# Kernel tuning notes

Hardware: AMD Instinct MI355X
Metric: run time of the kernel (lower is better)

## Reference

```python
import jax, jax.numpy as jnp
import numpy as np

NUM_EMBEDDINGS = 4096
EMBEDDING_DIM = 256
COMMITMENT_COST = 0.25
N_TOKENS = 32768


def setup_inputs() -> dict:
    key = jax.random.key(0)
    k1, k2 = jax.random.split(key)
    inputs = jax.random.normal(k1, (N_TOKENS, EMBEDDING_DIM), dtype=jnp.float32)
    # torch init: uniform(-1/K, 1/K)
    lim = 1.0 / NUM_EMBEDDINGS
    weight = jax.random.uniform(k2, (NUM_EMBEDDINGS, EMBEDDING_DIM), dtype=jnp.float32,
                                minval=-lim, maxval=lim)
    return {"inputs": inputs, "weight": weight}


def reference(inputs, weight):
    distances = (jnp.sum(inputs ** 2, axis=1, keepdims=True)
                 + jnp.sum(weight ** 2, axis=1)
                 - 2.0 * jnp.matmul(inputs, weight.T))
    encoding_indices = jnp.argmin(distances, axis=1)                       # [N]
    encodings = jax.nn.one_hot(encoding_indices, NUM_EMBEDDINGS,
                               dtype=jnp.float32)                          # [N, K]
    # gather replaces onehot @ weight (same values)
    quantized = weight[encoding_indices]                                   # [N, D]

    commitment_loss = jnp.mean((jax.lax.stop_gradient(quantized) - inputs) ** 2)
    codebook_loss = jnp.mean((quantized - jax.lax.stop_gradient(inputs)) ** 2)
    loss = codebook_loss + COMMITMENT_COST * commitment_loss

    # straight-through estimator
    quantized_st = inputs + jax.lax.stop_gradient(quantized - inputs)

    avg_probs = jnp.mean(encodings, axis=0)                                # [K]
    perplexity = jnp.exp(-jnp.sum(avg_probs * jnp.log(avg_probs + 1e-10)))

    return (quantized_st, perplexity, encodings, encoding_indices, loss)
```

## Files before the change

kernel.cpp:

```cpp
#include <hip/hip_runtime.h>

#define N_TOK 32768
#define N_EMB 4096
#define DIM 256
#define NSTEP 128

typedef short bf16x8 __attribute__((ext_vector_type(8)));
typedef float f32x4 __attribute__((ext_vector_type(4)));
typedef unsigned short us8 __attribute__((ext_vector_type(8)));


static __device__ __forceinline__ unsigned short f2bf(float f) {
    unsigned int u = __float_as_uint(f);
    u = (u + 0x7fffu + ((u >> 16) & 1u)) >> 16;
    return (unsigned short)u;
}

__device__ __forceinline__ float pw128_sq(const float4* a4) {
#pragma clang fp contract(off)
    float4 v0 = a4[0], v1 = a4[1];
    float r0 = v0.x * v0.x, r1 = v0.y * v0.y, r2 = v0.z * v0.z, r3 = v0.w * v0.w;
    float r4 = v1.x * v1.x, r5 = v1.y * v1.y, r6 = v1.z * v1.z, r7 = v1.w * v1.w;
    #pragma unroll
    for (int i = 1; i < 16; ++i) {
        v0 = a4[2 * i]; v1 = a4[2 * i + 1];
        float s;
        s = v0.x * v0.x; r0 += s;
        s = v0.y * v0.y; r1 += s;
        s = v0.z * v0.z; r2 += s;
        s = v0.w * v0.w; r3 += s;
        s = v1.x * v1.x; r4 += s;
        s = v1.y * v1.y; r5 += s;
        s = v1.z * v1.z; r6 += s;
        s = v1.w * v1.w; r7 += s;
    }
    return ((r0 + r1) + (r2 + r3)) + ((r4 + r5) + (r6 + r7));
}

__global__ __launch_bounds__(256) void k_prep_w(const float* __restrict__ w,
                                                unsigned short* __restrict__ Wh,
                                                float* __restrict__ e2_np) {
    const int T = blockIdx.x;
    const int t = threadIdx.x, lane = t & 63, g = t >> 6;
    #pragma unroll
    for (int cc = 0; cc < 2; ++cc) {
        int C = g * 2 + cc;
        int row = T * 16 + (lane & 15);
        int col = C * 32 + (lane >> 4) * 8;
        const float* s = w + (size_t)row * DIM + col;
        us8 h;
        #pragma unroll
        for (int j = 0; j < 8; ++j) h[j] = f2bf(s[j]);
        *(us8*)(Wh + ((size_t)(T * 8 + C) * 64 + lane) * 8) = h;
    }
    if (t < 16) {
        int row = T * 16 + t;
        const float4* a = (const float4*)(w + (size_t)row * DIM);
        float lo = pw128_sq(a);
        float hi = pw128_sq(a + 32);
        e2_np[row] = lo + hi;
    }
}

__global__ __launch_bounds__(256, 4) void k_score_mfma(
        const float* __restrict__ x, const float* __restrict__ w,
        const float* __restrict__ e2_np,
        const unsigned short* __restrict__ Wh,
        float* __restrict__ out_idx, unsigned int* __restrict__ counts,
        float* enc,
        float* __restrict__ outq, float* __restrict__ loss_acc) {
    __shared__ __align__(16) short Bbuf[2][8192];
    __shared__ float x2s[32];
    __shared__ float Tmax[2][32];
    __shared__ unsigned int ccnt[32];
    __shared__ int clist[32][16];
    __shared__ float Red_d[32 * 8];
    __shared__ int   Red_i[32 * 8];
    __shared__ float sred[4];

    const int t = threadIdx.x;
    const int wave = t >> 6, lane = t & 63;
    const int tok0 = blockIdx.x * 32;
    const int q = lane >> 4, c = lane & 15;
    const int mt = wave & 1, nb = wave >> 1;

    {
        const unsigned short* sp = Wh + (size_t)wave * 512 + lane * 8;
        #pragma unroll
        for (int k = 0; k < 4; ++k)
            __builtin_amdgcn_global_load_lds(
                (const __attribute__((address_space(1))) unsigned int*)(sp + k * 2048),
                (__attribute__((address_space(3))) unsigned int*)(&Bbuf[0][wave * 512 + k * 2048]),
                16, 0, 0);
    }

    bf16x8 ah[8];
    {
        const float* xrow = x + (size_t)(tok0 + mt * 16 + c) * DIM + q * 8;
        #pragma unroll
        for (int C = 0; C < 8; ++C) {
            float4 a = *(const float4*)(xrow + C * 32);
            float4 b = *(const float4*)(xrow + C * 32 + 4);
            us8 h;
            h[0] = f2bf(a.x); h[1] = f2bf(a.y); h[2] = f2bf(a.z); h[3] = f2bf(a.w);
            h[4] = f2bf(b.x); h[5] = f2bf(b.y); h[6] = f2bf(b.z); h[7] = f2bf(b.w);
            ah[C] = *(bf16x8*)&h;
        }
    }
    if (t < 32) {
        ccnt[t] = 0;
        const float4* a = (const float4*)(x + (size_t)(tok0 + t) * DIM);
        float lo = pw128_sq(a);
        float hi = pw128_sq(a + 32);
        x2s[t] = lo + hi;
    }
    __syncthreads();

    f32x4* ez = enc ? (f32x4*)(enc + (size_t)tok0 * N_EMB) : (f32x4*)0;
    const f32x4 zf4 = {0.f, 0.f, 0.f, 0.f};

    float vmax[4], v2[4];
    #pragma unroll
    for (int r = 0; r < 4; ++r) { vmax[r] = -3.4e38f; v2[r] = -3.4e38f; }
    for (int s = 0; s < NSTEP; ++s) {
        const int cur = s & 1;
        if (s + 1 < NSTEP) {
            const unsigned short* sp = Wh + (size_t)(s + 1) * 8192 + wave * 512 + lane * 8;
            short* dp = &Bbuf[cur ^ 1][wave * 512];
            #pragma unroll
            for (int k = 0; k < 4; ++k)
                __builtin_amdgcn_global_load_lds(
                    (const __attribute__((address_space(1))) unsigned int*)(sp + k * 2048),
                    (__attribute__((address_space(3))) unsigned int*)(dp + k * 2048),
                    16, 0, 0);
        }
        if (ez)
            __builtin_nontemporal_store(zf4, ez + s * 256 + t);

        f32x4 acc = {};
        #pragma unroll
        for (int C = 0; C < 8; ++C) {
            bf16x8 bh = *(const bf16x8*)(&Bbuf[cur][((nb * 8 + C) * 64 + lane) * 8]);
            acc = __builtin_amdgcn_mfma_f32_16x16x32_bf16(ah[C], bh, acc, 0, 0, 0);
        }
        #pragma unroll
        for (int r = 0; r < 4; ++r) {
            float p = __uint_as_float(
                (__float_as_uint(acc[r]) & ~127u) | (unsigned)s);
            if (p > vmax[r]) { v2[r] = vmax[r]; vmax[r] = p; }
            else if (p > v2[r]) v2[r] = p;
        }
        __syncthreads();
    }

    float rmax[4];
    #pragma unroll
    for (int r = 0; r < 4; ++r) rmax[r] = vmax[r];
    #pragma unroll
    for (int off = 1; off < 16; off <<= 1)
        #pragma unroll
        for (int r = 0; r < 4; ++r)
            rmax[r] = fmaxf(rmax[r], __shfl_xor(rmax[r], off));
    if (c == 0) {
        #pragma unroll
        for (int r = 0; r < 4; ++r)
            Tmax[nb][mt * 16 + q * 4 + r] = rmax[r];
    }
    __syncthreads();
    if (t < 32)
        Tmax[0][t] = fmaxf(Tmax[0][t], Tmax[1][t]) - 1.5e-4f;
    __syncthreads();
    float thr[4];
    #pragma unroll
    for (int r = 0; r < 4; ++r)
        thr[r] = Tmax[0][mt * 16 + q * 4 + r];

    #pragma unroll
    for (int r = 0; r < 4; ++r) {
        int tokl = mt * 16 + q * 4 + r;
        #pragma unroll
        for (int h = 0; h < 2; ++h) {
            float pv = h ? v2[r] : vmax[r];
            if (pv >= thr[r]) {
                int sid = (int)(__float_as_uint(pv) & 127u);
                int code = sid * 32 + nb * 16 + c;
                unsigned int p = atomicAdd(&ccnt[tokl], 1u);
                if (p < 16) clist[tokl][p] = code;
            }
        }
    }
    __syncthreads();

    {
        int token = t >> 3, slot = t & 7;
        int cnt = (int)ccnt[token]; if (cnt > 16) cnt = 16;
        float bd = 3.4e38f;
        int bi = 0x7fffffff;
        float x2 = x2s[token];
        const float4* xr = (const float4*)(x + (size_t)(tok0 + token) * DIM);
        for (int k = slot; k < cnt; k += 8) {
            int code = clist[token][k];
            const float4* wr = (const float4*)(w + (size_t)code * DIM);
            double dot = 0.0;
            for (int g = 0; g < 64; ++g) {
                float4 xv = xr[g];
                float4 wv = wr[g];
                dot += (double)xv.x * (double)wv.x;
                dot += (double)xv.y * (double)wv.y;
                dot += (double)xv.z * (double)wv.z;
                dot += (double)xv.w * (double)wv.w;
            }
            {
#pragma clang fp contract(off)
                float M  = (float)dot;
                float S  = x2 + e2_np[code];
                float dd = S - 2.0f * M;
                if (dd < bd || (dd == bd && code < bi)) { bd = dd; bi = code; }
            }
        }
        Red_d[token * 8 + slot] = bd;
        Red_i[token * 8 + slot] = bi;
    }
    __syncthreads();
    if (t < 32) {
        float fv = Red_d[t * 8];
        int   fi = Red_i[t * 8];
        #pragma unroll
        for (int k = 1; k < 8; ++k) {
            float v = Red_d[t * 8 + k];
            int  ii = Red_i[t * 8 + k];
            if (v < fv || (v == fv && ii < fi)) { fv = v; fi = ii; }
        }
        out_idx[tok0 + t] = (float)fi;
        atomicAdd(&counts[fi], 1u);
        ccnt[t] = (unsigned int)fi;
    }
    __syncthreads();

    {
        int token = t >> 3, slot = t & 7;
        int fi = (int)ccnt[token];
        if (enc && slot == 0)
            __builtin_nontemporal_store(1.0f, enc + (size_t)(tok0 + token) * N_EMB + fi);
        const f32x4* wr = (const f32x4*)(w + (size_t)fi * DIM);
        const f32x4* xr = (const f32x4*)(x + (size_t)(tok0 + token) * DIM);
        f32x4* oq = (f32x4*)(outq + (size_t)(tok0 + token) * DIM);
        float sse = 0.f;
        #pragma unroll
        for (int g0 = 0; g0 < 8; ++g0) {
            int g = slot * 8 + g0;
            f32x4 qv = wr[g];
            f32x4 xv = xr[g];
            __builtin_nontemporal_store(qv, oq + g);
            float dx = qv.x - xv.x, dy = qv.y - xv.y;
            float dz = qv.z - xv.z, dw = qv.w - xv.w;
            sse += dx * dx + dy * dy + dz * dz + dw * dw;
        }
        #pragma unroll
        for (int off = 32; off > 0; off >>= 1) sse += __shfl_down(sse, off, 64);
        if (lane == 0) sred[wave] = sse;
    }
    __syncthreads();
    if (t == 0)
        atomicAdd(loss_acc, sred[0] + sred[1] + sred[2] + sred[3]);
}

__global__ __launch_bounds__(256) void k_onehot(const float* __restrict__ out_idx,
                                                float* __restrict__ enc) {
    int token = blockIdx.x;
    int idx = (int)out_idx[token];
    float4* row = (float4*)(enc + (size_t)token * N_EMB);
    #pragma unroll
    for (int p = 0; p < 4; ++p) {
        int g = threadIdx.x + 256 * p;
        float4 v = make_float4(0.f, 0.f, 0.f, 0.f);
        int d0 = g * 4;
        if (idx >= d0 && idx < d0 + 4) ((float*)&v)[idx - d0] = 1.0f;
        row[g] = v;
    }
}

__global__ __launch_bounds__(256) void k_final(const unsigned int* __restrict__ counts,
                                               const float* __restrict__ loss_acc,
                                               float* __restrict__ out_perp,
                                               float* __restrict__ out_loss) {
    __shared__ float sred[4];
    int t = threadIdx.x;
    float h = 0.f;
    for (int k = t; k < N_EMB; k += 256) {
        float p = (float)counts[k] * (1.0f / N_TOK);
        h += p * logf(p + 1e-10f);
    }
    #pragma unroll
    for (int off = 32; off > 0; off >>= 1) h += __shfl_down(h, off, 64);
    if ((t & 63) == 0) sred[t >> 6] = h;
    __syncthreads();
    if (t == 0) {
        float s = sred[0] + sred[1] + sred[2] + sred[3];
        *out_perp = expf(-s);
        *out_loss = loss_acc[0] * 1.25f / 8388608.0f;
    }
}

extern "C" void kernel_launch(void* const* d_in, const int* in_sizes, int n_in,
                              void* d_out, int out_size, void* d_ws, size_t ws_size,
                              hipStream_t stream) {
    const float* x = (const float*)d_in[0];
    const float* w = (const float*)d_in[1];
    float* out  = (float*)d_out;
    float* out0 = out;
    float* out1 = out0 + 8388608;
    float* out2 = out1 + 1;
    float* out3 = out2 + 134217728;
    float* out4 = out3 + 32768;

    unsigned int* counts = (unsigned int*)d_ws;
    float* loss_acc = (float*)((char*)d_ws + 16384);
    float* e2_np    = (float*)((char*)d_ws + 16896);

    bool big_ws = ws_size >= (size_t)(20u * 1024u * 1024u);
    unsigned short* Wh;
    float* enc_arg;
    if (big_ws) {
        Wh = (unsigned short*)((char*)d_ws + 17u * 1024u * 1024u);
        enc_arg = out2;
    } else {
        uintptr_t sb = ((uintptr_t)out2 + 255) & ~(uintptr_t)255;
        Wh = (unsigned short*)sb;
        enc_arg = nullptr;
    }

    hipMemsetAsync(d_ws, 0, 16640, stream);
    k_prep_w<<<N_EMB / 16, 256, 0, stream>>>(w, Wh, e2_np);
    k_score_mfma<<<N_TOK / 32, 256, 0, stream>>>(x, w, e2_np, Wh,
                                                 out3, counts, enc_arg,
                                                 out0, loss_acc);
    if (!big_ws)
        k_onehot<<<N_TOK, 256, 0, stream>>>(out3, out2);
    k_final<<<1, 256, 0, stream>>>(counts, loss_acc, out1, out4);
}
```

Measured before the change: 685.8 us.

## Triple-buffer codebook tiles with single barrier and explicit vmcnt wait

Moves the LDS staging of bf16 codebook tiles from two buffers to three, so loads are issued two steps ahead. On the main path (encodings output present) it replaces the end-of-step __syncthreads with a partial s_waitcnt vmcnt(5) plus a raw barrier at the top of each step, letting the nontemporal zero stores stay outstanding. The aim is to hide global-load latency and stop the encoding stores from stalling the loop. To pay for the extra buffer's LDS, clist and the reduction arrays are aliased onto buffer 0. The risks are the hand-tuned vmcnt count being wrong and the redundant wrap-around prefetch loads.

```diff
diff --git a/kernel.cpp b/kernel.cpp
--- a/kernel.cpp
+++ b/kernel.cpp
@@ -69,14 +69,14 @@
         float* __restrict__ out_idx, unsigned int* __restrict__ counts,
         float* enc,
         float* __restrict__ outq, float* __restrict__ loss_acc) {
-    __shared__ __align__(16) short Bbuf[2][8192];
+    __shared__ __align__(16) short Bbuf[3][8192];
     __shared__ float x2s[32];
     __shared__ float Tmax[2][32];
     __shared__ unsigned int ccnt[32];
-    __shared__ int clist[32][16];
-    __shared__ float Red_d[32 * 8];
-    __shared__ int   Red_i[32 * 8];
     __shared__ float sred[4];
+    int*   clist = (int*)&Bbuf[0][0];
+    float* Red_d = (float*)&Bbuf[0][1024];
+    int*   Red_i = (int*)&Bbuf[0][1536];
 
     const int t = threadIdx.x;
     const int wave = t >> 6, lane = t & 63;
@@ -84,13 +84,15 @@
     const int q = lane >> 4, c = lane & 15;
     const int mt = wave & 1, nb = wave >> 1;
 
-    {
-        const unsigned short* sp = Wh + (size_t)wave * 512 + lane * 8;
+    #pragma unroll
+    for (int pb = 0; pb < 2; ++pb) {
+        const unsigned short* sp = Wh + (size_t)pb * 8192 + wave * 512 + lane * 8;
+        short* dp = &Bbuf[pb][wave * 512];
         #pragma unroll
         for (int k = 0; k < 4; ++k)
             __builtin_amdgcn_global_load_lds(
                 (const __attribute__((address_space(1))) unsigned int*)(sp + k * 2048),
-                (__attribute__((address_space(3))) unsigned int*)(&Bbuf[0][wave * 512 + k * 2048]),
+                (__attribute__((address_space(3))) unsigned int*)(dp + k * 2048),
                 16, 0, 0);
     }
 
@@ -122,35 +124,69 @@
     float vmax[4], v2[4];
     #pragma unroll
     for (int r = 0; r < 4; ++r) { vmax[r] = -3.4e38f; v2[r] = -3.4e38f; }
-    for (int s = 0; s < NSTEP; ++s) {
-        const int cur = s & 1;
-        if (s + 1 < NSTEP) {
-            const unsigned short* sp = Wh + (size_t)(s + 1) * 8192 + wave * 512 + lane * 8;
-            short* dp = &Bbuf[cur ^ 1][wave * 512];
+
+    short* pr = &Bbuf[0][0];
+    short* pn = &Bbuf[1][0];
+    short* ps = &Bbuf[2][0];
+
+    if (ez) {
+        for (int s = 0; s < NSTEP; ++s) {
+            asm volatile("s_waitcnt vmcnt(5)" ::: "memory");
+            __builtin_amdgcn_s_barrier();
+            __builtin_amdgcn_sched_barrier(0);
+            {
+                int ts = (s + 2) & 127;
+                const unsigned short* sp = Wh + (size_t)ts * 8192 + wave * 512 + lane * 8;
+                short* dp = ps + wave * 512;
+                #pragma unroll
+                for (int k = 0; k < 4; ++k)
+                    __builtin_amdgcn_global_load_lds(
+                        (const __attribute__((address_space(1))) unsigned int*)(sp + k * 2048),
+                        (__attribute__((address_space(3))) unsigned int*)(dp + k * 2048),
+                        16, 0, 0);
+            }
+            __builtin_nontemporal_store(zf4, ez + s * 256 + t);
+            f32x4 acc = {};
             #pragma unroll
-            for (int k = 0; k < 4; ++k)
-                __builtin_amdgcn_global_load_lds(
-                    (const __attribute__((address_space(1))) unsigned int*)(sp + k * 2048),
-                    (__attribute__((address_space(3))) unsigned int*)(dp + k * 2048),
-                    16, 0, 0);
-        }
-        if (ez)
-            __builtin_nontemporal_store(zf4, ez + s * 256 + t);
-
-        f32x4 acc = {};
-        #pragma unroll
-        for (int C = 0; C < 8; ++C) {
-            bf16x8 bh = *(const bf16x8*)(&Bbuf[cur][((nb * 8 + C) * 64 + lane) * 8]);
-            acc = __builtin_amdgcn_mfma_f32_16x16x32_bf16(ah[C], bh, acc, 0, 0, 0);
-        }
-        #pragma unroll
-        for (int r = 0; r < 4; ++r) {
-            float p = __uint_as_float(
-                (__float_as_uint(acc[r]) & ~127u) | (unsigned)s);
-            if (p > vmax[r]) { v2[r] = vmax[r]; vmax[r] = p; }
-            else if (p > v2[r]) v2[r] = p;
-        }
-        __syncthreads();
+            for (int C = 0; C < 8; ++C) {
+                bf16x8 bh = *(const bf16x8*)(pr + ((size_t)(nb * 8 + C) * 64 + lane) * 8);
+                acc = __builtin_amdgcn_mfma_f32_16x16x32_bf16(ah[C], bh, acc, 0, 0, 0);
+            }
+            #pragma unroll
+            for (int r = 0; r < 4; ++r) {
+                float p = __uint_as_float((__float_as_uint(acc[r]) & ~127u) | (unsigned)s);
+                if (p > vmax[r]) { v2[r] = vmax[r]; vmax[r] = p; }
+                else if (p > v2[r]) v2[r] = p;
+            }
+            short* tmp = pr; pr = pn; pn = ps; ps = tmp;
+        }
+    } else {
+        for (int s = 0; s < NSTEP; ++s) {
+            if (s + 2 < NSTEP) {
+                const unsigned short* sp = Wh + (size_t)(s + 2) * 8192 + wave * 512 + lane * 8;
+                short* dp = ps + wave * 512;
+                #pragma unroll
+                for (int k = 0; k < 4; ++k)
+                    __builtin_amdgcn_global_load_lds(
+                        (const __attribute__((address_space(1))) unsigned int*)(sp + k * 2048),
+                        (__attribute__((address_space(3))) unsigned int*)(dp + k * 2048),
+                        16, 0, 0);
+            }
+            f32x4 acc = {};
+            #pragma unroll
+            for (int C = 0; C < 8; ++C) {
+                bf16x8 bh = *(const bf16x8*)(pr + ((size_t)(nb * 8 + C) * 64 + lane) * 8);
+                acc = __builtin_amdgcn_mfma_f32_16x16x32_bf16(ah[C], bh, acc, 0, 0, 0);
+            }
+            #pragma unroll
+            for (int r = 0; r < 4; ++r) {
+                float p = __uint_as_float((__float_as_uint(acc[r]) & ~127u) | (unsigned)s);
+                if (p > vmax[r]) { v2[r] = vmax[r]; vmax[r] = p; }
+                else if (p > v2[r]) v2[r] = p;
+            }
+            __syncthreads();
+            short* tmp = pr; pr = pn; pn = ps; ps = tmp;
+        }
     }
 
     float rmax[4];
@@ -185,7 +221,7 @@
                 int sid = (int)(__float_as_uint(pv) & 127u);
                 int code = sid * 32 + nb * 16 + c;
                 unsigned int p = atomicAdd(&ccnt[tokl], 1u);
-                if (p < 16) clist[tokl][p] = code;
+                if (p < 16) clist[tokl * 16 + p] = code;
             }
         }
     }
@@ -199,7 +235,7 @@
         float x2 = x2s[token];
         const float4* xr = (const float4*)(x + (size_t)(tok0 + token) * DIM);
         for (int k = slot; k < cnt; k += 8) {
-            int code = clist[token][k];
+            int code = clist[token * 16 + k];
             const float4* wr = (const float4*)(w + (size_t)code * DIM);
             double dot = 0.0;
             for (int g = 0; g < 64; ++g) {
```

Measured after the change: 684.0 us. Within noise of the previous version (-0.3%).
